# Kernel optimization log

Measured on AMD Instinct MI355X. Metric: run time of the kernel, lower is better.

The kernel has to match this reference:

```python
import jax, jax.numpy as jnp
import numpy as np
from jax import lax

B, C, N, COUT, H, W = 8, 64, 16, 3, 96, 96
EPS = 1e-5  # torch GroupNorm / InstanceNorm2d default eps


def group_norm(x, gamma, beta, groups):
    n, c, h, w = x.shape
    xg = x.reshape(n, groups, c // groups, h, w)
    mu = xg.mean((2, 3, 4), keepdims=True)
    var = xg.var((2, 3, 4), keepdims=True)
    xg = (xg - mu) / jnp.sqrt(var + EPS)
    return xg.reshape(n, c, h, w) * gamma[None, :, None, None] + beta[None, :, None, None]


def instance_norm(x, gamma, beta):
    mu = x.mean((2, 3), keepdims=True)
    var = x.var((2, 3), keepdims=True)
    return (x - mu) / jnp.sqrt(var + EPS) * gamma[None, :, None, None] + beta[None, :, None, None]


def conv3x3(x, w, b):
    y = lax.conv_general_dilated(x, w, (1, 1), 'SAME',
                                 dimension_numbers=('NCHW', 'OIHW', 'NCHW'))
    return y + b[None, :, None, None]


def setup_inputs() -> dict:
    key = jax.random.key(0)
    ks = jax.random.split(key, 8)
    p = {}
    p['sr'] = jax.random.normal(ks[0], (B, C, H, W), jnp.float32)
    p['tg'] = jax.random.normal(ks[1], (B, C, H, W), jnp.float32)
    # self.w : Conv2d(c, c*n, 1) -> 1x1 conv == matmul over channels
    p['w_w'] = jax.random.normal(ks[2], (C * N, C), jnp.float32) * 0.05
    p['w_b'] = jnp.zeros((C * N,), jnp.float32)
    # mask_block: GN(c//4,c), ReLU, Conv(c,64,3), GN(16,64), ReLU, Conv(64,1,3)
    p['gn1_g'] = jnp.ones((C,), jnp.float32)
    p['gn1_b'] = jnp.zeros((C,), jnp.float32)
    p['c1_w'] = jax.random.normal(ks[3], (64, C, 3, 3), jnp.float32) * 0.05
    p['c1_b'] = jnp.zeros((64,), jnp.float32)
    p['gn2_g'] = jnp.ones((64,), jnp.float32)
    p['gn2_b'] = jnp.zeros((64,), jnp.float32)
    p['c2_w'] = jax.random.normal(ks[4], (1, 64, 3, 3), jnp.float32) * 0.05
    p['c2_b'] = jnp.zeros((1,), jnp.float32)
    # gen_block: IN(n), ReLU, Conv(n,n,1), IN(n), ReLU, Conv(n,cout,1)
    p['in1_g'] = jnp.ones((N,), jnp.float32)
    p['in1_b'] = jnp.zeros((N,), jnp.float32)
    p['c3_w'] = jax.random.normal(ks[5], (N, N), jnp.float32) * 0.1
    p['c3_b'] = jnp.zeros((N,), jnp.float32)
    p['in2_g'] = jnp.ones((N,), jnp.float32)
    p['in2_b'] = jnp.zeros((N,), jnp.float32)
    p['c4_w'] = jax.random.normal(ks[6], (COUT, N), jnp.float32) * 0.1
    p['c4_b'] = jnp.zeros((COUT,), jnp.float32)
    return p


def reference(sr, tg, w_w, w_b, gn1_g, gn1_b, c1_w, c1_b, gn2_g, gn2_b,
              c2_w, c2_b, in1_g, in1_b, c3_w, c3_b, in2_g, in2_b, c4_w, c4_b):
    b, c, h, w = sr.shape
    n = N
    # 1x1 conv then view to capsule layout [b, n, c, h*w]
    s = jnp.einsum('oc,bchw->bohw', w_w, sr) + w_b[None, :, None, None]
    s = s.reshape(b, n, c, h * w)
    op = s.sum(3, keepdims=True)  # [b,n,c,1]
    cof = None
    for _ in range(3):  # fixed 3-step dynamic routing
        opn = op / jnp.maximum(jnp.linalg.norm(op, axis=2, keepdims=True), 1e-12)
        cof = jax.nn.softmax((s * opn).sum(2, keepdims=True), axis=3)  # [b,n,1,hw]
        op = (s * cof).sum(3, keepdims=True)  # [b,n,c,1]
    # broadcast capsule vectors onto target feature map
    msk_tg = (tg[:, None, :, :, :] + op[:, :, :, :, None]).reshape(b * n, c, h, w)
    x = group_norm(msk_tg, gn1_g, gn1_b, c // 4)
    x = conv3x3(jax.nn.relu(x), c1_w, c1_b)
    x = group_norm(x, gn2_g, gn2_b, 64 // 4)
    x = conv3x3(jax.nn.relu(x), c2_w, c2_b)  # [b*n,1,h,w]
    msk = x.reshape(b, n, h, w)
    # spatial center-of-mass loss
    hw_cof = jax.nn.softmax(msk.reshape(b, n, h * w), -1).reshape(b, n, h, w)[..., None]
    hw_idx = jnp.stack(jnp.meshgrid(jnp.linspace(-1.0, 1.0, h),
                                    jnp.linspace(-1.0, 1.0, w), indexing='ij'), -1)[None, None]
    hw_centr = (hw_cof * hw_idx).sum((2, 3), keepdims=True)  # [b,n,1,1,2]
    centr_loss = (hw_cof * (hw_idx - hw_centr) ** 2).sum((2, 3, 4)).mean()
    # gen_block + sigmoid activation
    g = instance_norm(msk, in1_g, in1_b)
    g = jnp.einsum('on,bnhw->bohw', c3_w, jax.nn.relu(g)) + c3_b[None, :, None, None]
    g = instance_norm(g, in2_g, in2_b)
    rec = jax.nn.sigmoid(jnp.einsum('on,bnhw->bohw', c4_w, jax.nn.relu(g)) + c4_b[None, :, None, None])
    # outer product capsule x mask: [b,n,c,1] x [b,n,h,w] -> [b,n,c,h,w]
    op_out = jnp.einsum('bnc,bnhw->bnchw', op[..., 0], msk)
    return (op_out, msk, rec, centr_loss, cof.reshape(b, n, h, w))
```

## Files before the change

kernel.cpp:

```cpp
#include <hip/hip_runtime.h>
#include <math.h>

#define BB 8
#define CC 64
#define NCAP 16
#define HH 96
#define WW 96
#define PP (HH*WW)
#define BNN (BB*NCAP)
#define EPSN 1e-5f

typedef short short8 __attribute__((ext_vector_type(8)));
typedef unsigned short u16x8 __attribute__((ext_vector_type(8)));
typedef float float4v __attribute__((ext_vector_type(4)));

__device__ __forceinline__ float bf2f(unsigned short u){
  union{unsigned int i; float f;} x; x.i = ((unsigned int)u)<<16; return x.f;
}
__device__ __forceinline__ unsigned short f2bf(float f){
  union{float f; unsigned int i;} x; x.f=f;
  unsigned int r = x.i + 0x7fffu + ((x.i>>16)&1u);
  return (unsigned short)(r>>16);
}
__device__ __forceinline__ float4v mfma16(short8 a, short8 b, float4v c){
  return __builtin_amdgcn_mfma_f32_16x16x32_bf16(a, b, c, 0, 0, 0);
}

__device__ __forceinline__ float blkred_sum(float v, float* red4){
  int tid = threadIdx.x; int lane = tid & 63, wv = tid >> 6;
  #pragma unroll
  for (int off=32; off>0; off>>=1) v += __shfl_down(v, off, 64);
  __syncthreads();
  if (lane == 0) red4[wv] = v;
  __syncthreads();
  return red4[0] + red4[1] + red4[2] + red4[3];
}
__device__ __forceinline__ float blkred_max(float v, float* red4){
  int tid = threadIdx.x; int lane = tid & 63, wv = tid >> 6;
  #pragma unroll
  for (int off=32; off>0; off>>=1) v = fmaxf(v, __shfl_down(v, off, 64));
  __syncthreads();
  if (lane == 0) red4[wv] = v;
  __syncthreads();
  return fmaxf(fmaxf(red4[0], red4[1]), fmaxf(red4[2], red4[3]));
}

__global__ void kpre_tgt(const float* __restrict__ tg, unsigned short* __restrict__ tgt){
  int b = blockIdx.x/36, pc = blockIdx.x - (blockIdx.x/36)*36;
  int p = pc*256 + threadIdx.x;
  unsigned short vals[CC];
  #pragma unroll 8
  for (int c=0;c<CC;c++) vals[c] = f2bf(tg[((size_t)b*CC + c)*PP + p]);
  u16x8* dst = (u16x8*)&tgt[((size_t)b*PP + p)*CC];
  #pragma unroll
  for (int j=0;j<8;j++){
    u16x8 v;
    #pragma unroll
    for (int e=0;e<8;e++) v[e] = vals[j*8+e];
    dst[j] = v;
  }
}

__global__ void kw_bf16(const float* __restrict__ w1, unsigned short* __restrict__ Wt){
  int i = blockIdx.x*256 + threadIdx.x;
  int o = i/576; int rem = i - o*576; int c = rem/9; int tap = rem - c*9;
  Wt[(tap*CC + o)*CC + c] = f2bf(w1[i]);
}

__global__ void k0_colstats(const float* __restrict__ sr, const float* __restrict__ tg,
                            float* __restrict__ t, float* __restrict__ S1, float* __restrict__ S2){
  int row = blockIdx.x;
  const float* srp = sr + (size_t)row * PP;
  const float* tgp = tg + (size_t)row * PP;
  float s0=0.f, a1=0.f, a2=0.f;
  for (int p = threadIdx.x; p < PP; p += 256){
    s0 += srp[p];
    float v = tgp[p];
    a1 += v; a2 += v*v;
  }
  __shared__ float red4[4];
  s0 = blkred_sum(s0, red4);
  a1 = blkred_sum(a1, red4);
  a2 = blkred_sum(a2, red4);
  if (threadIdx.x == 0){ t[row]=s0; S1[row]=a1; S2[row]=a2; }
}

__global__ void k_update(const float* __restrict__ Wm, const float* __restrict__ wb,
                         const float* __restrict__ vec, float biasmul, int perB,
                         float* __restrict__ opv, float* __restrict__ uv, float* __restrict__ bu){
  int bn = blockIdx.x; int n = bn & (NCAP-1); int b = bn >> 4;
  int c = threadIdx.x;
  __shared__ float Wsh[CC*65];
  __shared__ float vsh[CC];
  __shared__ float opsh[CC];
  vsh[c] = perB ? vec[b*CC + c] : vec[bn*CC + c];
  const float* Wn = Wm + (size_t)n*CC*CC;
  for (int i=c;i<CC*CC;i+=64){ int r=i>>6, k=i&63; Wsh[r*65+k]=Wn[i]; }
  __syncthreads();
  float acc = biasmul * wb[n*CC + c];
  #pragma unroll 8
  for (int k=0;k<CC;k++) acc += Wsh[c*65+k]*vsh[k];
  opv[bn*CC+c] = acc;
  float ss = acc*acc;
  #pragma unroll
  for (int off=32;off>0;off>>=1) ss += __shfl_down(ss, off, 64);
  ss = __shfl(ss, 0, 64);
  float inv = 1.0f / fmaxf(sqrtf(ss), 1e-12f);
  opsh[c] = acc * inv;
  __syncthreads();
  float uacc = 0.f;
  #pragma unroll 8
  for (int k=0;k<CC;k++) uacc += opsh[k] * Wsh[k*65+c];
  uv[bn*CC+c] = uacc;
  float bb = opsh[c]*wb[n*CC+c];
  #pragma unroll
  for (int off=32;off>0;off>>=1) bb += __shfl_down(bb, off, 64);
  if (c==0) bu[bn] = bb;
}

__global__ __launch_bounds__(128) void k2f_dpass(
    const float* __restrict__ sr, const float* __restrict__ uv,
    const float* __restrict__ bu, float* __restrict__ dbuf,
    float* __restrict__ partm, float* __restrict__ partz,
    float* __restrict__ prt, int writed){
  int b = blockIdx.x / 72; int pc = blockIdx.x - b*72;
  int tid = threadIdx.x;
  int p = pc*128 + tid;
  __shared__ float ush[NCAP][CC];
  __shared__ float bush[NCAP];
  __shared__ float msh[NCAP];
  __shared__ float wsh[NCAP*132];
  __shared__ float srsh[CC*132];
  for (int i=tid;i<NCAP*CC;i+=128) ush[i>>6][i&63] = uv[b*NCAP*CC + i];
  if (tid < NCAP) bush[tid] = bu[b*NCAP+tid];
  __syncthreads();
  float acc[NCAP];
  #pragma unroll
  for (int n=0;n<NCAP;n++) acc[n]=bush[n];
  #pragma unroll 4
  for (int c=0;c<CC;c++){
    float v = sr[((size_t)b*CC + c)*PP + p];
    srsh[c*132+tid] = v;
    #pragma unroll
    for (int n=0;n<NCAP;n++) acc[n] += ush[n][c]*v;
  }
  #pragma unroll
  for (int n=0;n<NCAP;n++){
    wsh[n*132+tid] = acc[n];
    if (writed) dbuf[((size_t)(b*NCAP+n))*PP + p] = acc[n];
  }
  __syncthreads();
  {
    int n = tid >> 3, seg = tid & 7;
    float m = -1e30f;
    #pragma unroll
    for (int i=0;i<16;i++) m = fmaxf(m, wsh[n*132+seg*16+i]);
    #pragma unroll
    for (int off=1; off<8; off<<=1) m = fmaxf(m, __shfl_xor(m, off, 64));
    float z = 0.f;
    #pragma unroll
    for (int i=0;i<16;i++) z += __expf(wsh[n*132+seg*16+i] - m);
    #pragma unroll
    for (int off=1; off<8; off<<=1) z += __shfl_xor(z, off, 64);
    if (seg == 0){
      partm[(b*NCAP + n)*72 + pc] = m;
      partz[(b*NCAP + n)*72 + pc] = z;
      msh[n] = m;
    }
  }
  __syncthreads();
  #pragma unroll
  for (int n=0;n<NCAP;n++) wsh[n*132+tid] = __expf(wsh[n*132+tid]-msh[n]);
  __syncthreads();
  {
    int c = tid & 63, half = tid >> 6;
    float acc8[8];
    #pragma unroll
    for (int i=0;i<8;i++) acc8[i]=0.f;
    const float4* sp = (const float4*)&srsh[c*132];
    #pragma unroll 4
    for (int k=0;k<32;k++){
      float4 sv = sp[k];
      #pragma unroll
      for (int i=0;i<8;i++){
        float4 wv = *(const float4*)&wsh[(half*8+i)*132+4*k];
        acc8[i] += wv.x*sv.x + wv.y*sv.y + wv.z*sv.z + wv.w*sv.w;
      }
    }
    float* pb = prt + (((size_t)b*72+pc)*NCAP + half*8)*CC + c;
    #pragma unroll
    for (int i=0;i<8;i++) pb[(size_t)i*CC] = acc8[i];
  }
}

__global__ void k3b_combine(const float* __restrict__ partm, const float* __restrict__ partz,
                            float* __restrict__ mrow, float* __restrict__ zrow){
  int bn = blockIdx.x; int t = threadIdx.x;
  float m1 = partm[bn*72 + t];
  float m2 = (t < 8) ? partm[bn*72 + 64 + t] : -1e30f;
  float mm = fmaxf(m1, m2);
  #pragma unroll
  for (int off=32;off>0;off>>=1) mm = fmaxf(mm, __shfl_xor(mm, off, 64));
  float z = partz[bn*72 + t]*__expf(m1 - mm);
  if (t < 8) z += partz[bn*72 + 64 + t]*__expf(m2 - mm);
  #pragma unroll
  for (int off=32;off>0;off>>=1) z += __shfl_xor(z, off, 64);
  if (t==0){ mrow[bn]=mm; zrow[bn]=z; }
}

__global__ void k4c_combine(const float* __restrict__ prt, const float* __restrict__ partm,
                            const float* __restrict__ mrow, const float* __restrict__ zrow,
                            float* __restrict__ rv){
  int bn = blockIdx.x; int b = bn >> 4, n = bn & (NCAP-1);
  int c = threadIdx.x;
  float M = mrow[bn], invZ = 1.0f/zrow[bn];
  float s = 0.f;
  #pragma unroll 8
  for (int pc=0;pc<72;pc++){
    float w = __expf(partm[bn*72+pc] - M);
    s += prt[(((size_t)b*72+pc)*NCAP + n)*CC + c] * w;
  }
  rv[bn*CC+c] = s*invZ;
}

__global__ void k6_cofout(const float* __restrict__ dbuf, const float* __restrict__ mrow,
                          const float* __restrict__ zrow, float* __restrict__ cof){
  int bn = blockIdx.y;
  int p = blockIdx.x*256 + threadIdx.x;
  float m=mrow[bn], invz=1.0f/zrow[bn];
  cof[(size_t)bn*PP+p] = __expf(dbuf[(size_t)bn*PP+p]-m)*invz;
}

__global__ void k7_gn1(const float* __restrict__ S1, const float* __restrict__ S2,
                       const float* __restrict__ opv, const float* __restrict__ g1,
                       const float* __restrict__ b1, float* __restrict__ Aaff,
                       float* __restrict__ Daff, float* __restrict__ gn2s,
                       float* __restrict__ gn2q, float* __restrict__ in2s,
                       float* __restrict__ in2q){
  int bn = blockIdx.x; int b = bn >> 4;
  int c = threadIdx.x;
  __shared__ float e1[CC], e2[CC], mu[16], ri[16];
  float op = opv[bn*CC+c];
  float s1 = S1[b*CC+c], s2 = S2[b*CC+c];
  e1[c] = s1 + (float)PP*op;
  e2[c] = s2 + 2.0f*op*s1 + (float)PP*op*op;
  __syncthreads();
  if (c < 16){
    float m  = (e1[4*c]+e1[4*c+1]+e1[4*c+2]+e1[4*c+3])*(1.0f/(4.0f*PP));
    float qq = (e2[4*c]+e2[4*c+1]+e2[4*c+2]+e2[4*c+3])*(1.0f/(4.0f*PP));
    mu[c]=m; ri[c]=rsqrtf(qq-m*m+EPSN);
    gn2s[bn*16+c]=0.f; gn2q[bn*16+c]=0.f;
  }
  if (bn==0){ in2s[c]=0.f; in2s[CC+c]=0.f; in2q[c]=0.f; in2q[CC+c]=0.f; }
  __syncthreads();
  int g = c>>2;
  float A = ri[g]*g1[c];
  Aaff[bn*CC+c]=A;
  Daff[bn*CC+c]=(op-mu[g])*A + b1[c];
}

__global__ __launch_bounds__(256) void k8_conv1_mfma(
    const unsigned short* __restrict__ tgt, const unsigned short* __restrict__ Wt,
    const float* __restrict__ c1b, const float* __restrict__ Aaff,
    const float* __restrict__ Daff, unsigned short* __restrict__ y1b,
    float* __restrict__ gn2s, float* __restrict__ gn2q){
  int blk = blockIdx.x;
  int bn = blk/36, tt = blk - bn*36;
  int ty = tt/3, tx = tt - ty*3;
  int y0 = ty*8, x0 = tx*32;
  int b = bn >> 4;
  int tid = threadIdx.x, w = tid>>6, lane = tid&63, quad = lane>>4, col16 = lane&15;

  __shared__ unsigned short xh[10*34*72];
  __shared__ float Ash[CC], Dsh[CC];
  if (tid < CC){ Ash[tid]=Aaff[bn*CC+tid]; Dsh[tid]=Daff[bn*CC+tid]; }
  __syncthreads();

  const unsigned short* tgb = tgt + (size_t)b*PP*CC;
  for (int task = tid; task < 2720; task += 256){
    int j = task & 7, pi = task >> 3;
    int row = pi/34, col = pi - row*34;
    int gy = y0 + row - 1, gx = x0 + col - 1;
    u16x8 ov;
    if ((unsigned)gy < (unsigned)HH && (unsigned)gx < (unsigned)WW){
      u16x8 iv = *(const u16x8*)(tgb + ((size_t)(gy*WW+gx))*CC + j*8);
      #pragma unroll
      for (int e=0;e<8;e++){
        float f = bf2f(iv[e]);
        f = fmaxf(Ash[j*8+e]*f + Dsh[j*8+e], 0.f);
        ov[e] = f2bf(f);
      }
    } else {
      #pragma unroll
      for (int e=0;e<8;e++) ov[e]=0;
    }
    *(u16x8*)&xh[(row*34+col)*72 + j*8] = ov;
  }
  __syncthreads();

  float4v acc[4][4];
  #pragma unroll
  for (int mt=0;mt<4;mt++)
    #pragma unroll
    for (int nt=0;nt<4;nt++)
      #pragma unroll
      for (int e=0;e<4;e++) acc[mt][nt][e]=0.f;

  const unsigned short* xb0 = &xh[((2*w + 1)*34 + 1 + col16)*72 + quad*8];
  const unsigned short* wbase = Wt + (size_t)(col16*CC + quad*8);
  #pragma unroll
  for (int tap=0; tap<9; ++tap){
    const int dy = tap/3 - 1, dx = tap - (tap/3)*3 - 1;
    const int toff = (dy*34 + dx)*72;
    #pragma unroll
    for (int chunk=0; chunk<2; ++chunk){
      short8 a[4];
      #pragma unroll
      for (int mt=0;mt<4;mt++)
        a[mt] = *(const short8*)(wbase + tap*4096 + mt*1024 + chunk*32);
      short8 bf[4];
      #pragma unroll
      for (int nt=0;nt<4;nt++){
        int ri = nt>>1, h = nt&1;
        bf[nt] = *(const short8*)(xb0 + toff + ri*(34*72) + h*(16*72) + chunk*32);
      }
      #pragma unroll
      for (int mt=0;mt<4;mt++)
        #pragma unroll
        for (int nt=0;nt<4;nt++)
          acc[mt][nt] = mfma16(a[mt], bf[nt], acc[mt][nt]);
    }
  }

  unsigned short* ybn = y1b + (size_t)bn*CC*PP;
  #pragma unroll
  for (int mt=0;mt<4;mt++){
    float gs=0.f, gq=0.f;
    #pragma unroll
    for (int nt=0;nt<4;nt++){
      int ri = nt>>1, h = nt&1;
      int y = y0 + 2*w + ri, x = x0 + h*16 + col16;
      #pragma unroll
      for (int e=0;e<4;e++){
        int o = mt*16 + quad*4 + e;
        float v = acc[mt][nt][e] + c1b[o];
        ybn[(size_t)o*PP + y*WW + x] = f2bf(v);
        gs += v; gq += v*v;
      }
    }
    #pragma unroll
    for (int off=1; off<16; off<<=1){
      gs += __shfl_xor(gs, off, 64);
      gq += __shfl_xor(gq, off, 64);
    }
    if (col16==0){
      atomicAdd(&gn2s[bn*16 + mt*4 + quad], gs);
      atomicAdd(&gn2q[bn*16 + mt*4 + quad], gq);
    }
  }
}

__global__ void k9_gn2fin(const float* __restrict__ gn2s, const float* __restrict__ gn2q,
                          const float* __restrict__ g2c, const float* __restrict__ b2c,
                          float* __restrict__ A2, float* __restrict__ D2){
  int bn = blockIdx.x; int o = threadIdx.x;
  int g = o>>2;
  float m = gn2s[bn*16+g]*(1.0f/(4.0f*PP));
  float q = gn2q[bn*16+g]*(1.0f/(4.0f*PP));
  float ri = rsqrtf(q - m*m + EPSN);
  float A = ri * g2c[o];
  A2[bn*CC+o] = A;
  D2[bn*CC+o] = b2c[o] - m*A;
}

__global__ void k10_conv2(const unsigned short* __restrict__ y1b, const float* __restrict__ w2,
                          const float* __restrict__ b2, const float* __restrict__ A2,
                          const float* __restrict__ D2, float* __restrict__ mskout){
  int blk=blockIdx.x; int bn=blk/36; int tt=blk-bn*36;
  int y0=(tt/3)*8, x0=(tt%3)*32;
  int tid=threadIdx.x;
  int xi=tid&31, yi=tid>>5;
  __shared__ float xs[8][10][35];
  __shared__ float wsh2[CC*9];
  __shared__ float Ash[CC], Dsh[CC];
  for (int i=tid;i<CC*9;i+=256) wsh2[i]=w2[i];
  if (tid<CC){ Ash[tid]=A2[bn*CC+tid]; Dsh[tid]=D2[bn*CC+tid]; }
  float acc=0.f;
  const unsigned short* yb = y1b + (size_t)bn*CC*PP;
  #pragma unroll 1
  for (int cc2=0;cc2<CC;cc2+=8){
    __syncthreads();
    for (int i=tid;i<8*10*34;i+=256){
      int col=i%34; int rest=i/34; int row=rest%10; int ci=rest/10;
      int gy=y0+row-1, gx=x0+col-1;
      int cgl=cc2+ci;
      float v=0.f;
      if (gy>=0&&gy<HH&&gx>=0&&gx<WW)
        v=fmaxf(0.f, Ash[cgl]*bf2f(yb[(size_t)cgl*PP+gy*WW+gx])+Dsh[cgl]);
      xs[ci][row][col]=v;
    }
    __syncthreads();
    #pragma unroll 1
    for (int ci=0;ci<8;ci++){
      int cgl=cc2+ci;
      #pragma unroll
      for (int kh=0;kh<3;kh++){
        #pragma unroll
        for (int kw=0;kw<3;kw++)
          acc += wsh2[cgl*9+kh*3+kw]*xs[ci][yi+kh][xi+kw];
      }
    }
  }
  acc += b2[0];
  mskout[(size_t)bn*PP+(size_t)(y0+yi)*WW+(x0+xi)] = acc;
}

__global__ void k11_mskstats(const float* __restrict__ msk, const float* __restrict__ in1g,
                             const float* __restrict__ in1b, float* __restrict__ in1A,
                             float* __restrict__ in1D, float* __restrict__ lossbn){
  int bn = blockIdx.x; int n = bn & (NCAP-1);
  const float* mp = msk + (size_t)bn*PP;
  __shared__ float red4[4];
  float mx=-1e30f, s=0.f, q=0.f;
  for (int p=threadIdx.x;p<PP;p+=256){ float v=mp[p]; mx=fmaxf(mx,v); s+=v; q+=v*v; }
  mx = blkred_max(mx, red4);
  s  = blkred_sum(s, red4);
  q  = blkred_sum(q, red4);
  float z=0.f, sy=0.f, sx=0.f, syy=0.f, sxx=0.f;
  for (int p=threadIdx.x;p<PP;p+=256){
    float e = __expf(mp[p]-mx);
    int py = p/WW, px = p - py*WW;
    float iy = -1.0f + py*(2.0f/95.0f);
    float ix = -1.0f + px*(2.0f/95.0f);
    z+=e; sy+=e*iy; sx+=e*ix; syy+=e*iy*iy; sxx+=e*ix*ix;
  }
  z=blkred_sum(z,red4); sy=blkred_sum(sy,red4); sx=blkred_sum(sx,red4);
  syy=blkred_sum(syy,red4); sxx=blkred_sum(sxx,red4);
  if (threadIdx.x==0){
    float invz=1.0f/z;
    float ey=sy*invz, ex=sx*invz;
    lossbn[bn]=(syy*invz-ey*ey)+(sxx*invz-ex*ex);
    float mu=s*(1.0f/PP), var=q*(1.0f/PP)-mu*mu;
    float A=rsqrtf(var+EPSN)*in1g[n];
    in1A[bn]=A; in1D[bn]=in1b[n]-mu*A;
  }
}

__global__ void k12_loss(const float* __restrict__ lossbn, float* __restrict__ lossout){
  int tid=threadIdx.x;
  float v = lossbn[tid];
  #pragma unroll
  for (int off=32;off>0;off>>=1) v += __shfl_down(v,off,64);
  __shared__ float r2[2];
  if ((tid&63)==0) r2[tid>>6]=v;
  __syncthreads();
  if (tid==0) lossout[0] = (r2[0]+r2[1]) * (1.0f/128.0f);
}

__global__ void k13_gen1(const float* __restrict__ msk, const float* __restrict__ in1A,
                         const float* __restrict__ in1D, const float* __restrict__ c3w,
                         const float* __restrict__ c3b, float* __restrict__ g2,
                         float* __restrict__ in2s, float* __restrict__ in2q){
  int b = blockIdx.x/36; int pc = blockIdx.x - b*36;
  int p = pc*256+threadIdx.x;
  __shared__ float wsh[NCAP*NCAP];
  __shared__ float Ash[NCAP], Dsh[NCAP], bsh[NCAP];
  if (threadIdx.x < NCAP*NCAP) wsh[threadIdx.x] = c3w[threadIdx.x];
  if (threadIdx.x < NCAP){
    Ash[threadIdx.x]=in1A[b*NCAP+threadIdx.x];
    Dsh[threadIdx.x]=in1D[b*NCAP+threadIdx.x];
    bsh[threadIdx.x]=c3b[threadIdx.x];
  }
  __syncthreads();
  float h[NCAP];
  #pragma unroll
  for (int n=0;n<NCAP;n++)
    h[n] = fmaxf(0.f, Ash[n]*msk[(size_t)(b*NCAP+n)*PP+p] + Dsh[n]);
  float g[NCAP];
  #pragma unroll
  for (int o=0;o<NCAP;o++){
    float a = bsh[o];
    #pragma unroll
    for (int n=0;n<NCAP;n++) a += wsh[o*NCAP+n]*h[n];
    g[o]=a;
    g2[(size_t)(b*NCAP+o)*PP+p]=a;
  }
  int lane = threadIdx.x & 63;
  #pragma unroll
  for (int o=0;o<NCAP;o++){
    float a=g[o], q=g[o]*g[o];
    #pragma unroll
    for (int off=32;off>0;off>>=1){ a+=__shfl_down(a,off,64); q+=__shfl_down(q,off,64); }
    if (lane==0){ atomicAdd(&in2s[b*NCAP+o],a); atomicAdd(&in2q[b*NCAP+o],q); }
  }
}

__global__ void k14_in2fin(const float* __restrict__ in2s, const float* __restrict__ in2q,
                           const float* __restrict__ g, const float* __restrict__ bb,
                           float* __restrict__ in2A, float* __restrict__ in2D){
  int i=threadIdx.x;
  int o=i&15;
  float m=in2s[i]*(1.0f/PP), q=in2q[i]*(1.0f/PP);
  float A=rsqrtf(q-m*m+EPSN)*g[o];
  in2A[i]=A; in2D[i]=bb[o]-m*A;
}

__global__ void k15_rec(const float* __restrict__ g2, const float* __restrict__ in2A,
                        const float* __restrict__ in2D, const float* __restrict__ c4w,
                        const float* __restrict__ c4b, float* __restrict__ rec){
  int b = blockIdx.x/36; int pc = blockIdx.x - b*36;
  int p = pc*256+threadIdx.x;
  __shared__ float wsh[3*NCAP], Ash[NCAP], Dsh[NCAP], bsh[3];
  if (threadIdx.x<3*NCAP) wsh[threadIdx.x]=c4w[threadIdx.x];
  if (threadIdx.x<NCAP){ Ash[threadIdx.x]=in2A[b*NCAP+threadIdx.x]; Dsh[threadIdx.x]=in2D[b*NCAP+threadIdx.x]; }
  if (threadIdx.x<3) bsh[threadIdx.x]=c4b[threadIdx.x];
  __syncthreads();
  float h[NCAP];
  #pragma unroll
  for (int o=0;o<NCAP;o++)
    h[o]=fmaxf(0.f, Ash[o]*g2[(size_t)(b*NCAP+o)*PP+p]+Dsh[o]);
  #pragma unroll
  for (int j=0;j<3;j++){
    float z=bsh[j];
    #pragma unroll
    for (int o=0;o<NCAP;o++) z += wsh[j*NCAP+o]*h[o];
    rec[(size_t)(b*3+j)*PP+p] = 1.0f/(1.0f+__expf(-z));
  }
}

__global__ void k16_opout(const float* __restrict__ opv, const float* __restrict__ msk,
                          float* __restrict__ out){
  int bn = blockIdx.x / 9; int pt = blockIdx.x - bn*9;
  int base = pt*1024;
  __shared__ float ms[1024];
  __shared__ float opl[CC];
  for (int i=threadIdx.x;i<1024;i+=256) ms[i]=msk[(size_t)bn*PP+base+i];
  if (threadIdx.x<CC) opl[threadIdx.x]=opv[bn*CC+threadIdx.x];
  __syncthreads();
  float4 mv = ((const float4*)ms)[threadIdx.x];
  float* obase = out + (size_t)bn*CC*PP + base;
  #pragma unroll 4
  for (int c=0;c<CC;c++){
    float ov = opl[c];
    ((float4*)(obase + (size_t)c*PP))[threadIdx.x] = make_float4(ov*mv.x,ov*mv.y,ov*mv.z,ov*mv.w);
  }
}

extern "C" void kernel_launch(void* const* d_in, const int* in_sizes, int n_in,
                              void* d_out, int out_size, void* d_ws, size_t ws_size,
                              hipStream_t stream){
  const float* sr   = (const float*)d_in[0];
  const float* tg   = (const float*)d_in[1];
  const float* w_w  = (const float*)d_in[2];
  const float* w_b  = (const float*)d_in[3];
  const float* gn1g = (const float*)d_in[4];
  const float* gn1b = (const float*)d_in[5];
  const float* c1w  = (const float*)d_in[6];
  const float* c1b  = (const float*)d_in[7];
  const float* gn2g = (const float*)d_in[8];
  const float* gn2b = (const float*)d_in[9];
  const float* c2w  = (const float*)d_in[10];
  const float* c2b  = (const float*)d_in[11];
  const float* in1g = (const float*)d_in[12];
  const float* in1b = (const float*)d_in[13];
  const float* c3w  = (const float*)d_in[14];
  const float* c3b  = (const float*)d_in[15];
  const float* in2g = (const float*)d_in[16];
  const float* in2b = (const float*)d_in[17];
  const float* c4w  = (const float*)d_in[18];
  const float* c4b  = (const float*)d_in[19];
  float* out = (float*)d_out;
  float* ws  = (float*)d_ws;

  float* t_   = ws + 0;
  float* S1   = ws + 512;
  float* S2   = ws + 1024;
  float* opv  = ws + 1536;
  float* uv   = ws + 9728;
  float* bu   = ws + 17920;
  float* mrow = ws + 18048;
  float* zrow = ws + 18176;
  float* rv   = ws + 18304;
  float* Aaff = ws + 26496;
  float* Daff = ws + 34688;
  float* gn2s = ws + 42880;
  float* gn2q = ws + 44928;
  float* A2   = ws + 46976;
  float* D2   = ws + 55168;
  float* in1A = ws + 63360;
  float* in1D = ws + 63488;
  float* lossbn = ws + 63616;
  float* in2s = ws + 63744;
  float* in2q = ws + 63872;
  float* in2A = ws + 64000;
  float* in2D = ws + 64128;
  float* dbuf = ws + 65536;
  float* g2   = ws + 65536 + 1179648;

  unsigned short* y1b = (unsigned short*)d_out;
  unsigned short* tgt = (unsigned short*)((char*)d_out + 150994944);
  unsigned short* Wt  = (unsigned short*)((char*)d_out + 160432128);
  float* prt   = (float*)((char*)d_out + 160505856);
  float* partm = (float*)((char*)d_out + 162865152);
  float* partz = (float*)((char*)d_out + 162902016);
  float* mskout  = out + 75497472;
  float* recout  = out + 76677120;
  float* lossout = out + 76898304;
  float* cofout  = out + 76898305;

  kpre_tgt<<<BB*36, 256, 0, stream>>>(tg, tgt);
  kw_bf16<<<144, 256, 0, stream>>>(c1w, Wt);
  k0_colstats<<<BB*CC, 256, 0, stream>>>(sr, tg, t_, S1, S2);
  k_update<<<BNN, 64, 0, stream>>>(w_w, w_b, t_, (float)PP, 1, opv, uv, bu);
  for (int it=0; it<3; ++it){
    k2f_dpass<<<BB*72, 128, 0, stream>>>(sr, uv, bu, dbuf, partm, partz, prt, it==2 ? 1 : 0);
    k3b_combine<<<BNN, 64, 0, stream>>>(partm, partz, mrow, zrow);
    k4c_combine<<<BNN, 64, 0, stream>>>(prt, partm, mrow, zrow, rv);
    k_update<<<BNN, 64, 0, stream>>>(w_w, w_b, rv, 1.0f, 0, opv, uv, bu);
  }
  k6_cofout<<<dim3(36, BNN), 256, 0, stream>>>(dbuf, mrow, zrow, cofout);
  k7_gn1<<<BNN, 64, 0, stream>>>(S1, S2, opv, gn1g, gn1b, Aaff, Daff, gn2s, gn2q, in2s, in2q);
  k8_conv1_mfma<<<BNN*36, 256, 0, stream>>>(tgt, Wt, c1b, Aaff, Daff, y1b, gn2s, gn2q);
  k9_gn2fin<<<BNN, 64, 0, stream>>>(gn2s, gn2q, gn2g, gn2b, A2, D2);
  k10_conv2<<<BNN*36, 256, 0, stream>>>(y1b, c2w, c2b, A2, D2, mskout);
  k11_mskstats<<<BNN, 256, 0, stream>>>(mskout, in1g, in1b, in1A, in1D, lossbn);
  k12_loss<<<1, 128, 0, stream>>>(lossbn, lossout);
  k13_gen1<<<BB*36, 256, 0, stream>>>(mskout, in1A, in1D, c3w, c3b, g2, in2s, in2q);
  k14_in2fin<<<1, 128, 0, stream>>>(in2s, in2q, in2g, in2b, in2A, in2D);
  k15_rec<<<BB*36, 256, 0, stream>>>(g2, in2A, in2D, c4w, c4b, recout);
  k16_opout<<<BNN*9, 256, 0, stream>>>(opv, mskout, out);
}
```

Baseline: 1.074 ms.

## Store conv1 output channel-last and rewrite conv2 to consume NHWC tiles

The conv1 MFMA kernel now writes its bf16 output in pixel-major, channel-contiguous layout with 4-wide vector stores instead of channel-planar scalar stores. The conv2 kernel is rewritten to load one whole 64-channel halo tile with 16-byte vector loads, replacing the eight-pass staging loop with its repeated syncs. It now applies the GroupNorm affine and ReLU per tap while reading from LDS. Conv1 also gains software-pipelined register prefetch of the next MFMA operands and a min-occupancy launch bound. In exchange, conv2 redoes the affine+ReLU nine times per input and may hit LDS bank conflicts, and the occupancy hint may force register spills.

```diff
diff --git a/kernel.cpp b/kernel.cpp
--- a/kernel.cpp
+++ b/kernel.cpp
@@ -12,6 +12,7 @@
 
 typedef short short8 __attribute__((ext_vector_type(8)));
 typedef unsigned short u16x8 __attribute__((ext_vector_type(8)));
+typedef unsigned short u16x4 __attribute__((ext_vector_type(4)));
 typedef float float4v __attribute__((ext_vector_type(4)));
 
 __device__ __forceinline__ float bf2f(unsigned short u){
@@ -259,7 +260,7 @@
   Daff[bn*CC+c]=(op-mu[g])*A + b1[c];
 }
 
-__global__ __launch_bounds__(256) void k8_conv1_mfma(
+__global__ __launch_bounds__(256, 3) void k8_conv1_mfma(
     const unsigned short* __restrict__ tgt, const unsigned short* __restrict__ Wt,
     const float* __restrict__ c1b, const float* __restrict__ Aaff,
     const float* __restrict__ Daff, unsigned short* __restrict__ y1b,
@@ -308,31 +309,45 @@
 
   const unsigned short* xb0 = &xh[((2*w + 1)*34 + 1 + col16)*72 + quad*8];
   const unsigned short* wbase = Wt + (size_t)(col16*CC + quad*8);
-  #pragma unroll
-  for (int tap=0; tap<9; ++tap){
-    const int dy = tap/3 - 1, dx = tap - (tap/3)*3 - 1;
-    const int toff = (dy*34 + dx)*72;
-    #pragma unroll
-    for (int chunk=0; chunk<2; ++chunk){
-      short8 a[4];
+
+  short8 a_c[4], b_c[4];
+  {
+    const int toff0 = ((0/3 - 1)*34 + (0%3) - 1)*72;
+    #pragma unroll
+    for (int mt=0;mt<4;mt++) a_c[mt] = *(const short8*)(wbase + 0*4096 + mt*1024);
+    #pragma unroll
+    for (int nt=0;nt<4;nt++){
+      int ri = nt>>1, h = nt&1;
+      b_c[nt] = *(const short8*)(xb0 + toff0 + ri*2448 + h*1152);
+    }
+  }
+  #pragma unroll
+  for (int s=0; s<18; ++s){
+    short8 a_n[4], b_n[4];
+    if (s < 17){
+      const int s1 = s+1, tap1 = s1>>1, ch1 = s1&1;
+      const int toff1 = ((tap1/3 - 1)*34 + (tap1%3) - 1)*72;
       #pragma unroll
       for (int mt=0;mt<4;mt++)
-        a[mt] = *(const short8*)(wbase + tap*4096 + mt*1024 + chunk*32);
-      short8 bf[4];
+        a_n[mt] = *(const short8*)(wbase + tap1*4096 + mt*1024 + ch1*32);
       #pragma unroll
       for (int nt=0;nt<4;nt++){
         int ri = nt>>1, h = nt&1;
-        bf[nt] = *(const short8*)(xb0 + toff + ri*(34*72) + h*(16*72) + chunk*32);
+        b_n[nt] = *(const short8*)(xb0 + toff1 + ri*2448 + h*1152 + ch1*32);
       }
-      #pragma unroll
-      for (int mt=0;mt<4;mt++)
-        #pragma unroll
-        for (int nt=0;nt<4;nt++)
-          acc[mt][nt] = mfma16(a[mt], bf[nt], acc[mt][nt]);
-    }
-  }
-
-  unsigned short* ybn = y1b + (size_t)bn*CC*PP;
+    }
+    #pragma unroll
+    for (int mt=0;mt<4;mt++)
+      #pragma unroll
+      for (int nt=0;nt<4;nt++)
+        acc[mt][nt] = mfma16(a_c[mt], b_c[nt], acc[mt][nt]);
+    if (s < 17){
+      #pragma unroll
+      for (int i=0;i<4;i++){ a_c[i]=a_n[i]; b_c[i]=b_n[i]; }
+    }
+  }
+
+  unsigned short* ybn = y1b + (size_t)bn*PP*CC;
   #pragma unroll
   for (int mt=0;mt<4;mt++){
     float gs=0.f, gq=0.f;
@@ -340,13 +355,15 @@
     for (int nt=0;nt<4;nt++){
       int ri = nt>>1, h = nt&1;
       int y = y0 + 2*w + ri, x = x0 + h*16 + col16;
+      u16x4 pv;
       #pragma unroll
       for (int e=0;e<4;e++){
         int o = mt*16 + quad*4 + e;
         float v = acc[mt][nt][e] + c1b[o];
-        ybn[(size_t)o*PP + y*WW + x] = f2bf(v);
+        pv[e] = f2bf(v);
         gs += v; gq += v*v;
       }
+      *(u16x4*)&ybn[(size_t)(y*WW + x)*CC + mt*16 + quad*4] = pv;
     }
     #pragma unroll
     for (int off=1; off<16; off<<=1){
@@ -373,46 +390,56 @@
   D2[bn*CC+o] = b2c[o] - m*A;
 }
 
-__global__ void k10_conv2(const unsigned short* __restrict__ y1b, const float* __restrict__ w2,
-                          const float* __restrict__ b2, const float* __restrict__ A2,
-                          const float* __restrict__ D2, float* __restrict__ mskout){
+__global__ __launch_bounds__(256) void k10_conv2(
+    const unsigned short* __restrict__ y1b, const float* __restrict__ w2,
+    const float* __restrict__ b2, const float* __restrict__ A2,
+    const float* __restrict__ D2, float* __restrict__ mskout){
   int blk=blockIdx.x; int bn=blk/36; int tt=blk-bn*36;
   int y0=(tt/3)*8, x0=(tt%3)*32;
   int tid=threadIdx.x;
-  int xi=tid&31, yi=tid>>5;
-  __shared__ float xs[8][10][35];
+  __shared__ unsigned short xh2[10*34*72];
   __shared__ float wsh2[CC*9];
   __shared__ float Ash[CC], Dsh[CC];
   for (int i=tid;i<CC*9;i+=256) wsh2[i]=w2[i];
   if (tid<CC){ Ash[tid]=A2[bn*CC+tid]; Dsh[tid]=D2[bn*CC+tid]; }
-  float acc=0.f;
-  const unsigned short* yb = y1b + (size_t)bn*CC*PP;
-  #pragma unroll 1
-  for (int cc2=0;cc2<CC;cc2+=8){
-    __syncthreads();
-    for (int i=tid;i<8*10*34;i+=256){
-      int col=i%34; int rest=i/34; int row=rest%10; int ci=rest/10;
-      int gy=y0+row-1, gx=x0+col-1;
-      int cgl=cc2+ci;
-      float v=0.f;
-      if (gy>=0&&gy<HH&&gx>=0&&gx<WW)
-        v=fmaxf(0.f, Ash[cgl]*bf2f(yb[(size_t)cgl*PP+gy*WW+gx])+Dsh[cgl]);
-      xs[ci][row][col]=v;
-    }
-    __syncthreads();
-    #pragma unroll 1
-    for (int ci=0;ci<8;ci++){
-      int cgl=cc2+ci;
-      #pragma unroll
-      for (int kh=0;kh<3;kh++){
+
+  const unsigned short* yb = y1b + (size_t)bn*PP*CC;
+  for (int task=tid; task<2720; task+=256){
+    int j = task & 7, pi = task >> 3;
+    int row = pi/34, col = pi - row*34;
+    int gy = y0 + row - 1, gx = x0 + col - 1;
+    u16x8 iv;
+    if ((unsigned)gy < (unsigned)HH && (unsigned)gx < (unsigned)WW){
+      iv = *(const u16x8*)(yb + ((size_t)(gy*WW+gx))*CC + j*8);
+    } else {
+      #pragma unroll
+      for (int e=0;e<8;e++) iv[e]=0;
+    }
+    *(u16x8*)&xh2[(row*34+col)*72 + j*8] = iv;
+  }
+  __syncthreads();
+
+  int xi = tid&31, yi = tid>>5;
+  float acc = 0.f;
+  for (int t=0; t<9; ++t){
+    int kh = t/3, kw = t - kh*3;
+    int gy2 = y0 + yi + kh - 1, gx2 = x0 + xi + kw - 1;
+    if ((unsigned)gy2 < (unsigned)HH && (unsigned)gx2 < (unsigned)WW){
+      const unsigned short* px = &xh2[((yi+kh)*34 + xi+kw)*72];
+      #pragma unroll
+      for (int oct=0; oct<8; ++oct){
+        u16x8 v = *(const u16x8*)(px + oct*8);
         #pragma unroll
-        for (int kw=0;kw<3;kw++)
-          acc += wsh2[cgl*9+kh*3+kw]*xs[ci][yi+kh][xi+kw];
+        for (int e=0;e<8;e++){
+          int c = oct*8 + e;
+          float xv = fmaxf(Ash[c]*bf2f(v[e]) + Dsh[c], 0.f);
+          acc += wsh2[c*9 + t] * xv;
+        }
       }
     }
   }
   acc += b2[0];
-  mskout[(size_t)bn*PP+(size_t)(y0+yi)*WW+(x0+xi)] = acc;
+  mskout[(size_t)bn*PP + (size_t)(y0+yi)*WW + (x0+xi)] = acc;
 }
 
 __global__ void k11_mskstats(const float* __restrict__ msk, const float* __restrict__ in1g,
```

New measurement: 1.037 ms. 1.04x faster.
